# Optimization experiments

Measured on AMD Instinct MI355X. Metric: run time of the kernel, lower is better.

The kernel has to match this reference:

```python
import jax, jax.numpy as jnp
import numpy as np
from jax import lax

WIN = 7
K1, K2 = 0.01, 0.03
NP_ = WIN * WIN
COV_NORM = NP_ / (NP_ - 1)


def _box_filter(t, w):
    # t: [B, C, H, W] -> valid 7x7 box mean, [B, C, H-6, W-6]
    B, C, H, W = t.shape
    o = lax.conv_general_dilated(
        t.reshape(B * C, 1, H, W), w, window_strides=(1, 1), padding='VALID',
        dimension_numbers=('NCHW', 'OIHW', 'NCHW'))
    return o.reshape(B, C, H - WIN + 1, W - WIN + 1)


def setup_inputs() -> dict:
    key = jax.random.key(0)
    kx, ky = jax.random.split(key)
    X = jax.random.uniform(kx, (32, 3, 512, 512), dtype=jnp.float32)
    Y = jax.random.uniform(ky, (32, 3, 512, 512), dtype=jnp.float32)
    return {"X": X, "Y": Y}


def reference(X, Y):
    data_range = 1.0
    C1 = (K1 * data_range) ** 2
    C2 = (K2 * data_range) ** 2
    w = jnp.full((1, 1, WIN, WIN), 1.0 / NP_, dtype=X.dtype)

    ux = _box_filter(X, w)
    uy = _box_filter(Y, w)
    uxx = _box_filter(X * X, w)
    uyy = _box_filter(Y * Y, w)
    uxy = _box_filter(X * Y, w)

    vx = COV_NORM * (uxx - ux * ux)
    vy = COV_NORM * (uyy - uy * uy)
    vxy = COV_NORM * (uxy - ux * uy)

    A1 = 2 * ux * uy + C1
    A2 = 2 * vxy + C2
    B1 = ux * ux + uy * uy + C1
    B2 = vx + vy + C2
    S = (A1 * A2) / (B1 * B2)
    # reduced=True: per-channel means then mean over channels == global mean
    # (all channels have identical spatial size)
    return 1.0 - jnp.mean(S)
```

## Files before the change

kernel.cpp:

```cpp
#include <hip/hip_runtime.h>


#define IW    512
#define OUTW  506
#define OUTH  506
#define BAND  46
#define NBANDS 11
#define NIMG  96
#define C1N2  0.2401f
#define C2N2  2.1609f
#define KA    (49.0f/24.0f)
#define KB    (49.0f/48.0f)
#define TOTAL_OUT 24579456.0f

__global__ void ssim_zero(float* acc) {
    if (threadIdx.x == 0) acc[0] = 0.0f;
}

__global__ __launch_bounds__(128) void ssim_main(const float* __restrict__ X,
                                                 const float* __restrict__ Y,
                                                 float* __restrict__ acc) {
    __shared__ float plane[2][5][65 * 12];

    const int t    = threadIdx.x;
    const int band = blockIdx.x;
    const int img  = blockIdx.y;
    const int r0   = band * BAND;
    const float4* X4 = (const float4*)(X + (size_t)img * IW * IW);
    const float4* Y4 = (const float4*)(Y + (size_t)img * IW * IW);

    float4 s0 = {0,0,0,0}, s1 = {0,0,0,0}, s2 = {0,0,0,0},
           s3 = {0,0,0,0}, s4 = {0,0,0,0};

#pragma unroll
    for (int i = 0; i < 6; ++i) {
        float4 x = X4[(r0 + i) * 128 + t];
        float4 y = Y4[(r0 + i) * 128 + t];
        s0.x += x.x; s0.y += x.y; s0.z += x.z; s0.w += x.w;
        s1.x += y.x; s1.y += y.y; s1.z += y.z; s1.w += y.w;
        s2.x = fmaf(x.x,x.x,s2.x); s2.y = fmaf(x.y,x.y,s2.y);
        s2.z = fmaf(x.z,x.z,s2.z); s2.w = fmaf(x.w,x.w,s2.w);
        s3.x = fmaf(y.x,y.x,s3.x); s3.y = fmaf(y.y,y.y,s3.y);
        s3.z = fmaf(y.z,y.z,s3.z); s3.w = fmaf(y.w,y.w,s3.w);
        s4.x = fmaf(x.x,y.x,s4.x); s4.y = fmaf(x.y,y.y,s4.y);
        s4.z = fmaf(x.z,y.z,s4.z); s4.w = fmaf(x.w,y.w,s4.w);
    }

    const int wslot = 12 * (t >> 1) + 4 * (t & 1);
    const int wv = t >> 6;
    const int s  = t & 63;
    float accS = 0.0f;

    for (int j = 0; j < BAND; j += 2) {
#pragma unroll
        for (int k = 0; k < 2; ++k) {
            const int rr = r0 + j + k;
            float4 x = X4[(rr + 6) * 128 + t];
            float4 y = Y4[(rr + 6) * 128 + t];
            s0.x += x.x; s0.y += x.y; s0.z += x.z; s0.w += x.w;
            s1.x += y.x; s1.y += y.y; s1.z += y.z; s1.w += y.w;
            s2.x = fmaf(x.x,x.x,s2.x); s2.y = fmaf(x.y,x.y,s2.y);
            s2.z = fmaf(x.z,x.z,s2.z); s2.w = fmaf(x.w,x.w,s2.w);
            s3.x = fmaf(y.x,y.x,s3.x); s3.y = fmaf(y.y,y.y,s3.y);
            s3.z = fmaf(y.z,y.z,s3.z); s3.w = fmaf(y.w,y.w,s3.w);
            s4.x = fmaf(x.x,y.x,s4.x); s4.y = fmaf(x.y,y.y,s4.y);
            s4.z = fmaf(x.z,y.z,s4.z); s4.w = fmaf(x.w,y.w,s4.w);
            *(float4*)&plane[k][0][wslot] = s0;
            *(float4*)&plane[k][1][wslot] = s1;
            *(float4*)&plane[k][2][wslot] = s2;
            *(float4*)&plane[k][3][wslot] = s3;
            *(float4*)&plane[k][4][wslot] = s4;
            float4 ox = X4[rr * 128 + t];
            float4 oy = Y4[rr * 128 + t];
            s0.x -= ox.x; s0.y -= ox.y; s0.z -= ox.z; s0.w -= ox.w;
            s1.x -= oy.x; s1.y -= oy.y; s1.z -= oy.z; s1.w -= oy.w;
            s2.x = fmaf(-ox.x,ox.x,s2.x); s2.y = fmaf(-ox.y,ox.y,s2.y);
            s2.z = fmaf(-ox.z,ox.z,s2.z); s2.w = fmaf(-ox.w,ox.w,s2.w);
            s3.x = fmaf(-oy.x,oy.x,s3.x); s3.y = fmaf(-oy.y,oy.y,s3.y);
            s3.z = fmaf(-oy.z,oy.z,s3.z); s3.w = fmaf(-oy.w,oy.w,s3.w);
            s4.x = fmaf(-ox.x,oy.x,s4.x); s4.y = fmaf(-ox.y,oy.y,s4.y);
            s4.z = fmaf(-ox.z,oy.z,s4.z); s4.w = fmaf(-ox.w,oy.w,s4.w);
        }
        __syncthreads();

        float W[5][8];
#pragma unroll
        for (int q = 0; q < 5; ++q) {
            const float* pl = plane[wv][q];
            float4 a = *(const float4*)(pl + 12 * s);
            float4 b = *(const float4*)(pl + 12 * s + 4);
            float4 cc = *(const float4*)(pl + 12 * (s + 1));
            float2 dd = *(const float2*)(pl + 12 * (s + 1) + 4);
            float c[14] = {a.x, a.y, a.z, a.w, b.x, b.y, b.z, b.w,
                           cc.x, cc.y, cc.z, cc.w, dd.x, dd.y};
            float Wv = ((c[0] + c[1]) + (c[2] + c[3])) +
                       ((c[4] + c[5]) + c[6]);
            W[q][0] = Wv;
#pragma unroll
            for (int m = 1; m < 8; ++m) {
                Wv += c[m + 6] - c[m - 1];
                W[q][m] = Wv;
            }
        }
#pragma unroll
        for (int m = 0; m < 8; ++m) {
            float Sx = W[0][m], Sy = W[1][m];
            float Sxx = W[2][m], Syy = W[3][m], Sxy = W[4][m];
            float sxsy = Sx * Sy;
            float p    = fmaf(Sx, Sx, Sy * Sy);
            float a1   = fmaf(2.0f, sxsy, C1N2);
            float b1   = p + C1N2;
            float t1   = fmaf(49.0f, Sxy, -sxsy);
            float a2   = fmaf(KA, t1, C2N2);
            float qq   = Sxx + Syy;
            float t2   = fmaf(49.0f, qq, -p);
            float b2   = fmaf(KB, t2, C2N2);
            float num  = a1 * a2;
            float den  = b1 * b2;
            float S    = num * __builtin_amdgcn_rcpf(den);
            accS += (8 * s + m < OUTW) ? S : 0.0f;
        }
        __syncthreads();
    }

#pragma unroll
    for (int off = 32; off > 0; off >>= 1)
        accS += __shfl_down(accS, off, 64);
    __shared__ float wsum[2];
    if (s == 0) wsum[wv] = accS;
    __syncthreads();
    if (t == 0) atomicAdd(acc, wsum[0] + wsum[1]);
}

__global__ void ssim_finalize(const float* __restrict__ acc,
                              float* __restrict__ out) {
    if (threadIdx.x == 0) out[0] = 1.0f - acc[0] / TOTAL_OUT;
}

extern "C" void kernel_launch(void* const* d_in, const int* in_sizes, int n_in,
                              void* d_out, int out_size, void* d_ws, size_t ws_size,
                              hipStream_t stream) {
    const float* X = (const float*)d_in[0];
    const float* Y = (const float*)d_in[1];
    float* accum = (float*)d_ws;
    float* out = (float*)d_out;

    hipLaunchKernelGGL(ssim_zero, dim3(1), dim3(64), 0, stream, accum);
    hipLaunchKernelGGL(ssim_main, dim3(NBANDS, NIMG), dim3(128), 0, stream,
                       X, Y, accum);
    hipLaunchKernelGGL(ssim_finalize, dim3(1), dim3(64), 0, stream, accum, out);
}
```

Before: 248.5 us.

## Give each wavefront its own 11-row band with register halo shuffles

Each 64-lane wavefront now handles its own 11-row band of one image, and each lane owns 8 columns. The horizontal 7-tap window is completed with cross-lane shuffles of the column sums instead of a shared-memory staging plane guarded by block barriers. This removes all LDS traffic and __syncthreads, raises the number of independent work units, and software-prefetches the next entering and leaving rows. In exchange, shorter bands re-read more of the 6-row vertical halo, each lane needs more registers, and there are many more atomics to the single accumulator.

```diff
diff --git a/kernel.cpp b/kernel.cpp
--- a/kernel.cpp
+++ b/kernel.cpp
@@ -3,10 +3,10 @@
 
 #define IW    512
 #define OUTW  506
-#define OUTH  506
-#define BAND  46
-#define NBANDS 11
+#define RBAND 11
+#define NB    46
 #define NIMG  96
+#define NWAVE (NIMG * NB)
 #define C1N2  0.2401f
 #define C2N2  2.1609f
 #define KA    (49.0f/24.0f)
@@ -17,119 +17,128 @@
     if (threadIdx.x == 0) acc[0] = 0.0f;
 }
 
-__global__ __launch_bounds__(128) void ssim_main(const float* __restrict__ X,
+__device__ __forceinline__ float ssim_raw(float Sx, float Sy, float Sxx,
+                                          float Syy, float Sxy) {
+    float sxsy = Sx * Sy;
+    float p    = fmaf(Sx, Sx, Sy * Sy);
+    float a1   = fmaf(2.0f, sxsy, C1N2);
+    float b1   = p + C1N2;
+    float a2   = fmaf(KA, fmaf(49.0f, Sxy, -sxsy), C2N2);
+    float b2   = fmaf(KB, fmaf(49.0f, Sxx + Syy, -p), C2N2);
+    return (a1 * a2) * __builtin_amdgcn_rcpf(b1 * b2);
+}
+
+__device__ __forceinline__ void acc_add(float cs[5][8],
+                                        const float4& xa, const float4& xb,
+                                        const float4& ya, const float4& yb) {
+    float xs[8] = {xa.x, xa.y, xa.z, xa.w, xb.x, xb.y, xb.z, xb.w};
+    float ys[8] = {ya.x, ya.y, ya.z, ya.w, yb.x, yb.y, yb.z, yb.w};
+#pragma unroll
+    for (int c = 0; c < 8; ++c) {
+        cs[0][c] += xs[c];
+        cs[1][c] += ys[c];
+        cs[2][c] = fmaf(xs[c], xs[c], cs[2][c]);
+        cs[3][c] = fmaf(ys[c], ys[c], cs[3][c]);
+        cs[4][c] = fmaf(xs[c], ys[c], cs[4][c]);
+    }
+}
+
+__device__ __forceinline__ void acc_sub(float cs[5][8],
+                                        const float4& xa, const float4& xb,
+                                        const float4& ya, const float4& yb) {
+    float xs[8] = {xa.x, xa.y, xa.z, xa.w, xb.x, xb.y, xb.z, xb.w};
+    float ys[8] = {ya.x, ya.y, ya.z, ya.w, yb.x, yb.y, yb.z, yb.w};
+#pragma unroll
+    for (int c = 0; c < 8; ++c) {
+        cs[0][c] -= xs[c];
+        cs[1][c] -= ys[c];
+        cs[2][c] = fmaf(-xs[c], xs[c], cs[2][c]);
+        cs[3][c] = fmaf(-ys[c], ys[c], cs[3][c]);
+        cs[4][c] = fmaf(-xs[c], ys[c], cs[4][c]);
+    }
+}
+
+__global__ __launch_bounds__(256) void ssim_main(const float* __restrict__ X,
                                                  const float* __restrict__ Y,
                                                  float* __restrict__ acc) {
-    __shared__ float plane[2][5][65 * 12];
+    const int t  = threadIdx.x;
+    const int s  = t & 63;
+    const int w  = blockIdx.x * 4 + (t >> 6);
+    const int img  = w / NB;
+    const int band = w % NB;
+    const int r0 = band * RBAND;
 
-    const int t    = threadIdx.x;
-    const int band = blockIdx.x;
-    const int img  = blockIdx.y;
-    const int r0   = band * BAND;
     const float4* X4 = (const float4*)(X + (size_t)img * IW * IW);
     const float4* Y4 = (const float4*)(Y + (size_t)img * IW * IW);
+    const int ci = 2 * s;
 
-    float4 s0 = {0,0,0,0}, s1 = {0,0,0,0}, s2 = {0,0,0,0},
-           s3 = {0,0,0,0}, s4 = {0,0,0,0};
+    float cs[5][8];
+#pragma unroll
+    for (int q = 0; q < 5; ++q)
+#pragma unroll
+        for (int c = 0; c < 8; ++c) cs[q][c] = 0.0f;
 
 #pragma unroll
     for (int i = 0; i < 6; ++i) {
-        float4 x = X4[(r0 + i) * 128 + t];
-        float4 y = Y4[(r0 + i) * 128 + t];
-        s0.x += x.x; s0.y += x.y; s0.z += x.z; s0.w += x.w;
-        s1.x += y.x; s1.y += y.y; s1.z += y.z; s1.w += y.w;
-        s2.x = fmaf(x.x,x.x,s2.x); s2.y = fmaf(x.y,x.y,s2.y);
-        s2.z = fmaf(x.z,x.z,s2.z); s2.w = fmaf(x.w,x.w,s2.w);
-        s3.x = fmaf(y.x,y.x,s3.x); s3.y = fmaf(y.y,y.y,s3.y);
-        s3.z = fmaf(y.z,y.z,s3.z); s3.w = fmaf(y.w,y.w,s3.w);
-        s4.x = fmaf(x.x,y.x,s4.x); s4.y = fmaf(x.y,y.y,s4.y);
-        s4.z = fmaf(x.z,y.z,s4.z); s4.w = fmaf(x.w,y.w,s4.w);
+        const int r = r0 + i;
+        float4 xa = X4[r * 128 + ci], xb = X4[r * 128 + ci + 1];
+        float4 ya = Y4[r * 128 + ci], yb = Y4[r * 128 + ci + 1];
+        acc_add(cs, xa, xb, ya, yb);
     }
 
-    const int wslot = 12 * (t >> 1) + 4 * (t & 1);
-    const int wv = t >> 6;
-    const int s  = t & 63;
+    float4 nxa = X4[(r0 + 6) * 128 + ci], nxb = X4[(r0 + 6) * 128 + ci + 1];
+    float4 nya = Y4[(r0 + 6) * 128 + ci], nyb = Y4[(r0 + 6) * 128 + ci + 1];
+    float4 rxa = X4[r0 * 128 + ci],       rxb = X4[r0 * 128 + ci + 1];
+    float4 rya = Y4[r0 * 128 + ci],       ryb = Y4[r0 * 128 + ci + 1];
+
     float accS = 0.0f;
 
-    for (int j = 0; j < BAND; j += 2) {
+    for (int j = 0; j < RBAND; ++j) {
+        acc_add(cs, nxa, nxb, nya, nyb);
+
+        {
+            const int rn = min(r0 + j + 7, IW - 1);
+            nxa = X4[rn * 128 + ci]; nxb = X4[rn * 128 + ci + 1];
+            nya = Y4[rn * 128 + ci]; nyb = Y4[rn * 128 + ci + 1];
+        }
+
+        float halo[5][6];
 #pragma unroll
-        for (int k = 0; k < 2; ++k) {
-            const int rr = r0 + j + k;
-            float4 x = X4[(rr + 6) * 128 + t];
-            float4 y = Y4[(rr + 6) * 128 + t];
-            s0.x += x.x; s0.y += x.y; s0.z += x.z; s0.w += x.w;
-            s1.x += y.x; s1.y += y.y; s1.z += y.z; s1.w += y.w;
-            s2.x = fmaf(x.x,x.x,s2.x); s2.y = fmaf(x.y,x.y,s2.y);
-            s2.z = fmaf(x.z,x.z,s2.z); s2.w = fmaf(x.w,x.w,s2.w);
-            s3.x = fmaf(y.x,y.x,s3.x); s3.y = fmaf(y.y,y.y,s3.y);
-            s3.z = fmaf(y.z,y.z,s3.z); s3.w = fmaf(y.w,y.w,s3.w);
-            s4.x = fmaf(x.x,y.x,s4.x); s4.y = fmaf(x.y,y.y,s4.y);
-            s4.z = fmaf(x.z,y.z,s4.z); s4.w = fmaf(x.w,y.w,s4.w);
-            *(float4*)&plane[k][0][wslot] = s0;
-            *(float4*)&plane[k][1][wslot] = s1;
-            *(float4*)&plane[k][2][wslot] = s2;
-            *(float4*)&plane[k][3][wslot] = s3;
-            *(float4*)&plane[k][4][wslot] = s4;
-            float4 ox = X4[rr * 128 + t];
-            float4 oy = Y4[rr * 128 + t];
-            s0.x -= ox.x; s0.y -= ox.y; s0.z -= ox.z; s0.w -= ox.w;
-            s1.x -= oy.x; s1.y -= oy.y; s1.z -= oy.z; s1.w -= oy.w;
-            s2.x = fmaf(-ox.x,ox.x,s2.x); s2.y = fmaf(-ox.y,ox.y,s2.y);
-            s2.z = fmaf(-ox.z,ox.z,s2.z); s2.w = fmaf(-ox.w,ox.w,s2.w);
-            s3.x = fmaf(-oy.x,oy.x,s3.x); s3.y = fmaf(-oy.y,oy.y,s3.y);
-            s3.z = fmaf(-oy.z,oy.z,s3.z); s3.w = fmaf(-oy.w,oy.w,s3.w);
-            s4.x = fmaf(-ox.x,oy.x,s4.x); s4.y = fmaf(-ox.y,oy.y,s4.y);
-            s4.z = fmaf(-ox.z,oy.z,s4.z); s4.w = fmaf(-ox.w,oy.w,s4.w);
+        for (int q = 0; q < 5; ++q)
+#pragma unroll
+            for (int k = 0; k < 6; ++k)
+                halo[q][k] = __shfl_down(cs[q][k], 1, 64);
+
+        float W[5];
+#pragma unroll
+        for (int q = 0; q < 5; ++q)
+            W[q] = ((cs[q][0] + cs[q][1]) + (cs[q][2] + cs[q][3])) +
+                   ((cs[q][4] + cs[q][5]) + cs[q][6]);
+        accS += ssim_raw(W[0], W[1], W[2], W[3], W[4]);
+#pragma unroll
+        for (int m = 1; m < 8; ++m) {
+#pragma unroll
+            for (int q = 0; q < 5; ++q) {
+                float cn = (m == 1) ? cs[q][7] : halo[q][m - 2];
+                W[q] += cn - cs[q][m - 1];
+            }
+            float Sv = ssim_raw(W[0], W[1], W[2], W[3], W[4]);
+            if (m < 2) accS += Sv;
+            else       accS += (8 * s + m < OUTW) ? Sv : 0.0f;
         }
-        __syncthreads();
 
-        float W[5][8];
-#pragma unroll
-        for (int q = 0; q < 5; ++q) {
-            const float* pl = plane[wv][q];
-            float4 a = *(const float4*)(pl + 12 * s);
-            float4 b = *(const float4*)(pl + 12 * s + 4);
-            float4 cc = *(const float4*)(pl + 12 * (s + 1));
-            float2 dd = *(const float2*)(pl + 12 * (s + 1) + 4);
-            float c[14] = {a.x, a.y, a.z, a.w, b.x, b.y, b.z, b.w,
-                           cc.x, cc.y, cc.z, cc.w, dd.x, dd.y};
-            float Wv = ((c[0] + c[1]) + (c[2] + c[3])) +
-                       ((c[4] + c[5]) + c[6]);
-            W[q][0] = Wv;
-#pragma unroll
-            for (int m = 1; m < 8; ++m) {
-                Wv += c[m + 6] - c[m - 1];
-                W[q][m] = Wv;
-            }
+        acc_sub(cs, rxa, rxb, rya, ryb);
+        {
+            const int rr = r0 + j + 1;
+            rxa = X4[rr * 128 + ci]; rxb = X4[rr * 128 + ci + 1];
+            rya = Y4[rr * 128 + ci]; ryb = Y4[rr * 128 + ci + 1];
         }
-#pragma unroll
-        for (int m = 0; m < 8; ++m) {
-            float Sx = W[0][m], Sy = W[1][m];
-            float Sxx = W[2][m], Syy = W[3][m], Sxy = W[4][m];
-            float sxsy = Sx * Sy;
-            float p    = fmaf(Sx, Sx, Sy * Sy);
-            float a1   = fmaf(2.0f, sxsy, C1N2);
-            float b1   = p + C1N2;
-            float t1   = fmaf(49.0f, Sxy, -sxsy);
-            float a2   = fmaf(KA, t1, C2N2);
-            float qq   = Sxx + Syy;
-            float t2   = fmaf(49.0f, qq, -p);
-            float b2   = fmaf(KB, t2, C2N2);
-            float num  = a1 * a2;
-            float den  = b1 * b2;
-            float S    = num * __builtin_amdgcn_rcpf(den);
-            accS += (8 * s + m < OUTW) ? S : 0.0f;
-        }
-        __syncthreads();
     }
 
 #pragma unroll
     for (int off = 32; off > 0; off >>= 1)
         accS += __shfl_down(accS, off, 64);
-    __shared__ float wsum[2];
-    if (s == 0) wsum[wv] = accS;
-    __syncthreads();
-    if (t == 0) atomicAdd(acc, wsum[0] + wsum[1]);
+    if (s == 0) atomicAdd(acc, accS);
 }
 
 __global__ void ssim_finalize(const float* __restrict__ acc,
@@ -146,7 +155,7 @@
     float* out = (float*)d_out;
 
     hipLaunchKernelGGL(ssim_zero, dim3(1), dim3(64), 0, stream, accum);
-    hipLaunchKernelGGL(ssim_main, dim3(NBANDS, NIMG), dim3(128), 0, stream,
+    hipLaunchKernelGGL(ssim_main, dim3(NWAVE / 4), dim3(256), 0, stream,
                        X, Y, accum);
     hipLaunchKernelGGL(ssim_finalize, dim3(1), dim3(64), 0, stream, accum, out);
 }
```

Result: slower. 265.7 us (+6.9%).
